# Kernel tuning notes

Measured on AMD Instinct MI355X. Metric: run time of the kernel, lower is better.

The kernel has to match this reference:

```python
import jax, jax.numpy as jnp
import numpy as np

N, C, T, V = 128, 256, 48, 25
CR = C // 16
SEG = 3
BN_EPS = 1e-5


def setup_inputs() -> dict:
    key = jax.random.key(0)
    ks = jax.random.split(key, 8)
    s = lambda k, shape: jax.random.normal(k, shape, dtype=jnp.float32) * 0.05
    return {
        "x": jax.random.normal(ks[0], (N, C, T, V), dtype=jnp.float32),
        "w_sq": s(ks[1], (CR, C)),   # me_squeeze 1x1 conv weight [out,in]
        "b_sq": s(ks[2], (CR,)),
        "gamma": jnp.ones((CR,), jnp.float32),   # BN weight
        "beta": jnp.zeros((CR,), jnp.float32),   # BN bias
        "rmean": jnp.zeros((CR,), jnp.float32),  # BN running mean
        "rvar": jnp.ones((CR,), jnp.float32),    # BN running var
        "w_c1": s(ks[3], (CR, CR)),  # me_conv1 1x1 conv weight
        "b_c1": s(ks[4], (CR,)),
        "w_ex": s(ks[5], (C, CR)),   # me_expand 1x1 conv weight
        "b_ex": s(ks[6], (C,)),
    }


def reference(x, w_sq, b_sq, gamma, beta, rmean, rvar, w_c1, b_c1, w_ex, b_ex):
    n, c, t, v = x.shape
    nb = (n * t) // SEG
    cr = w_sq.shape[0]
    # 1x1 squeeze conv + BatchNorm (eval mode, running stats) -> [n, cr, t, v]
    y = jnp.einsum('nctv,rc->nrtv', x, w_sq) + b_sq[None, :, None, None]
    scale = gamma / jnp.sqrt(rvar + BN_EPS)
    y = y * scale[None, :, None, None] + (beta - rmean * scale)[None, :, None, None]
    # 1x1 conv on squeezed features (shifted branch)
    y1 = jnp.einsum('nrtv,sr->nstv', y, w_c1) + b_c1[None, :, None, None]
    # regroup consecutive frames into segments of SEG along time: (n*t) -> (nb, SEG)
    yseg = y.transpose(0, 2, 1, 3).reshape(nb, SEG, cr, v)
    y1seg = y1.transpose(0, 2, 1, 3).reshape(nb, SEG, cr, v)
    # temporal difference: conv(frame k+1) - frame k, zero-pad last frame of each segment
    diff = y1seg[:, 1:] - yseg[:, :SEG - 1]                    # [nb, SEG-1, cr, v]
    diff = jnp.pad(diff, ((0, 0), (0, 1), (0, 0), (0, 0)))     # [nb, SEG, cr, v]
    x_me = diff.reshape(n, t, cr, v).transpose(0, 2, 1, 3)     # [n, cr, t, v]
    # adaptive avg pool over joints (v -> 1), expand conv, sigmoid gate
    m = jnp.mean(x_me, axis=-1, keepdims=True)                 # [n, cr, t, 1]
    gate = jax.nn.sigmoid(jnp.einsum('nrtu,cr->nctu', m, w_ex) + b_ex[None, :, None, None])
    return x * gate
```

## Files before the change

kernel.cpp:

```cpp
#include <hip/hip_runtime.h>

#define N_  128
#define C_  256
#define T_  48
#define V_  25

typedef float v4f __attribute__((ext_vector_type(4)));

__global__ __launch_bounds__(256) void k_rowmean(const float* __restrict__ x,
                                                 float* __restrict__ xbar) {
    __shared__ float xs[6400];
    const int tid = threadIdx.x;
    const float4* x4 = (const float4*)x;
    const unsigned base4 = blockIdx.x * 1600u;
    #pragma unroll
    for (int k = 0; k < 7; ++k) {
        int i4 = k * 256 + tid;
        if (i4 < 1600) ((float4*)xs)[i4] = x4[base4 + i4];
    }
    __syncthreads();
    float s = 0.f;
    #pragma unroll
    for (int v = 0; v < 25; ++v) s += xs[tid * 25 + v];
    xbar[blockIdx.x * 256u + tid] = s * 0.04f;
}

__global__ __launch_bounds__(512, 4) void k_gateapply(
    const float* __restrict__ x, const float* __restrict__ xbar,
    const float* __restrict__ wsq, const float* __restrict__ bsq,
    const float* __restrict__ gamma, const float* __restrict__ beta,
    const float* __restrict__ rmean, const float* __restrict__ rvar,
    const float* __restrict__ wc1, const float* __restrict__ bc1,
    const float* __restrict__ wex, const float* __restrict__ bex,
    float* __restrict__ out)
{
    __shared__ float xm[12 * 256];
    __shared__ float wsqL[256 * 17];
    __shared__ float gs[256 * 12];
    __shared__ float part[384];
    __shared__ float ybn[192], y1[192], mv[192];

    const int tid = threadIdx.x;
    const unsigned bid = blockIdx.x;
    const unsigned o  = (bid & 7u) * 64u + (bid >> 3);
    const unsigned n  = o >> 2;
    const unsigned qd = o & 3u;

    for (int j = tid; j < 3072; j += 512) {
        int c = j / 12, t = j - c * 12;
        xm[t * 256 + c] = xbar[(unsigned)((n * 256u + c) * 48u + qd * 12u + t)];
    }
    #pragma unroll
    for (int it = 0; it < 8; ++it) {
        int j = it * 512 + tid;
        int r = j >> 8, c = j & 255;
        wsqL[c * 17 + r] = wsq[j];
    }
    __syncthreads();

    if (tid < 384) {
        int t = tid >> 5, rh = tid & 31, r = rh >> 1, h = rh & 1;
        float acc = 0.f;
        #pragma unroll 8
        for (int i = 0; i < 128; ++i)
            acc += xm[t * 256 + h * 128 + i] * wsqL[(h * 128 + i) * 17 + r];
        part[tid] = acc;
    }
    __syncthreads();
    if (tid < 192) {
        int t = tid >> 4, r = tid & 15;
        float acc = part[t * 32 + r * 2] + part[t * 32 + r * 2 + 1];
        float sc = gamma[r] * rsqrtf(rvar[r] + 1e-5f);
        ybn[t * 16 + r] = (acc + bsq[r]) * sc + (beta[r] - rmean[r] * sc);
    }
    __syncthreads();
    if (tid < 192) {
        int t = tid >> 4, s = tid & 15;
        float acc = bc1[s];
        #pragma unroll
        for (int r = 0; r < 16; ++r) acc += ybn[t * 16 + r] * wc1[s * 16 + r];
        y1[t * 16 + s] = acc;
    }
    __syncthreads();
    if (tid < 192) {
        int t = tid >> 4, r = tid & 15;
        mv[tid] = ((t % 3) < 2) ? (y1[(t + 1) * 16 + r] - ybn[t * 16 + r]) : 0.f;
    }
    __syncthreads();
    {
        int c = tid & 255, half = tid >> 8;
        float wexr[16];
        #pragma unroll
        for (int r = 0; r < 16; ++r) wexr[r] = wex[c * 16 + r];
        float be = bex[c];
        #pragma unroll
        for (int t = half * 6; t < half * 6 + 6; ++t) {
            float a = be;
            #pragma unroll
            for (int r = 0; r < 16; ++r) a += mv[t * 16 + r] * wexr[r];
            gs[c * 12 + t] = 1.f / (1.f + expf(-a));
        }
    }
    __syncthreads();

    const v4f* x4 = (const v4f*)x + (size_t)n * 76800u + qd * 75u;
    v4f*       o4 = (v4f*)out     + (size_t)n * 76800u + qd * 75u;
    #pragma unroll 4
    for (int it = 0; it < 38; ++it) {
        int j = it * 512 + tid;
        if (j < 19200) {
            unsigned c = ((unsigned)j * 55926u) >> 22;
            int k = j - (int)c * 75;
            v4f v = x4[c * 300 + k];
            int m0  = k * 4;
            int t0  = (m0 * 41) >> 10;
            int t3  = ((m0 + 3) * 41) >> 10;
            int rem = m0 - t0 * 25;
            float g0 = gs[c * 12 + t0];
            float g3 = gs[c * 12 + t3];
            v4f ov;
            ov.x = v.x * g0;
            ov.y = v.y * ((rem + 1 < 25) ? g0 : g3);
            ov.z = v.z * ((rem + 2 < 25) ? g0 : g3);
            ov.w = v.w * ((rem + 3 < 25) ? g0 : g3);
            __builtin_nontemporal_store(ov, &o4[c * 300 + k]);
        }
    }
}

extern "C" void kernel_launch(void* const* d_in, const int* in_sizes, int n_in,
                              void* d_out, int out_size, void* d_ws, size_t ws_size,
                              hipStream_t stream) {
    const float* x     = (const float*)d_in[0];
    const float* wsq   = (const float*)d_in[1];
    const float* bsq   = (const float*)d_in[2];
    const float* gamma = (const float*)d_in[3];
    const float* beta  = (const float*)d_in[4];
    const float* rmean = (const float*)d_in[5];
    const float* rvar  = (const float*)d_in[6];
    const float* wc1   = (const float*)d_in[7];
    const float* bc1   = (const float*)d_in[8];
    const float* wex   = (const float*)d_in[9];
    const float* bex   = (const float*)d_in[10];

    float* xbar = (float*)d_ws;

    k_rowmean<<<6144, 256, 0, stream>>>(x, xbar);
    k_gateapply<<<512, 512, 0, stream>>>(x, xbar, wsq, bsq, gamma, beta,
                                         rmean, rvar, wc1, bc1, wex, bex,
                                         (float*)d_out);
}
```

Measured before the change: 87.40 us.

## Fuse row-mean and gate-apply into one cooperative kernel with grid sync

Replaces the separate row-mean and gate-apply kernels with a single cooperative kernel of 512 blocks. Each block first computes the joint means for six chunks of x, then a grid-wide sync precedes the original gate computation and apply. Shared memory moves to a dynamic 51200-byte buffer that both phases reuse. This removes one kernel launch and the gap between launches. In exchange it adds a grid barrier, and the 50 KB of shared memory per block may limit how many blocks fit on each CU.

After: 147.4 us. 68.7% more time.

```diff
diff --git a/kernel.cpp b/kernel.cpp
--- a/kernel.cpp
+++ b/kernel.cpp
@@ -1,48 +1,57 @@
 #include <hip/hip_runtime.h>
+#include <hip/hip_cooperative_groups.h>
 
 #define N_  128
 #define C_  256
 #define T_  48
 #define V_  25
 
+namespace cg = cooperative_groups;
 typedef float v4f __attribute__((ext_vector_type(4)));
 
-__global__ __launch_bounds__(256) void k_rowmean(const float* __restrict__ x,
-                                                 float* __restrict__ xbar) {
-    __shared__ float xs[6400];
-    const int tid = threadIdx.x;
-    const float4* x4 = (const float4*)x;
-    const unsigned base4 = blockIdx.x * 1600u;
-    #pragma unroll
-    for (int k = 0; k < 7; ++k) {
-        int i4 = k * 256 + tid;
-        if (i4 < 1600) ((float4*)xs)[i4] = x4[base4 + i4];
-    }
-    __syncthreads();
-    float s = 0.f;
-    #pragma unroll
-    for (int v = 0; v < 25; ++v) s += xs[tid * 25 + v];
-    xbar[blockIdx.x * 256u + tid] = s * 0.04f;
-}
-
-__global__ __launch_bounds__(512, 4) void k_gateapply(
-    const float* __restrict__ x, const float* __restrict__ xbar,
+__global__ __launch_bounds__(512, 4) void k_coop(
+    const float* __restrict__ x,
     const float* __restrict__ wsq, const float* __restrict__ bsq,
     const float* __restrict__ gamma, const float* __restrict__ beta,
     const float* __restrict__ rmean, const float* __restrict__ rvar,
     const float* __restrict__ wc1, const float* __restrict__ bc1,
     const float* __restrict__ wex, const float* __restrict__ bex,
-    float* __restrict__ out)
+    float* __restrict__ xbar, float* __restrict__ out)
 {
-    __shared__ float xm[12 * 256];
-    __shared__ float wsqL[256 * 17];
-    __shared__ float gs[256 * 12];
-    __shared__ float part[384];
-    __shared__ float ybn[192], y1[192], mv[192];
-
+    extern __shared__ float S[];
     const int tid = threadIdx.x;
     const unsigned bid = blockIdx.x;
-    const unsigned o  = (bid & 7u) * 64u + (bid >> 3);
+    const unsigned o   = (bid & 7u) * 64u + (bid >> 3);
+
+    {
+        const v4f* x4 = (const v4f*)x;
+        float* xs = S;
+        for (int ch = 0; ch < 6; ++ch) {
+            const unsigned g4 = (o * 6u + ch) * 3200u;
+            #pragma unroll
+            for (int i = 0; i < 7; ++i) {
+                int j = i * 512 + tid;
+                if (j < 3200) ((v4f*)xs)[j] = x4[g4 + j];
+            }
+            __syncthreads();
+            const float* row = xs + tid * 25;
+            float s = 0.f;
+            #pragma unroll
+            for (int v = 0; v < 25; ++v) s += row[v];
+            xbar[(o * 6u + ch) * 512u + tid] = s * 0.04f;
+            __syncthreads();
+        }
+    }
+    cg::this_grid().sync();
+
+    float* xm   = S;
+    float* wsqL = S + 3072;
+    float* gs   = S + 7424;
+    float* part = S + 10496;
+    float* ybn  = S + 10880;
+    float* y1   = S + 11072;
+    float* mv   = S + 11264;
+
     const unsigned n  = o >> 2;
     const unsigned qd = o & 3u;
 
@@ -103,27 +112,29 @@
     }
     __syncthreads();
 
-    const v4f* x4 = (const v4f*)x + (size_t)n * 76800u + qd * 75u;
-    v4f*       o4 = (v4f*)out     + (size_t)n * 76800u + qd * 75u;
-    #pragma unroll 4
-    for (int it = 0; it < 38; ++it) {
-        int j = it * 512 + tid;
-        if (j < 19200) {
-            unsigned c = ((unsigned)j * 55926u) >> 22;
-            int k = j - (int)c * 75;
-            v4f v = x4[c * 300 + k];
-            int m0  = k * 4;
-            int t0  = (m0 * 41) >> 10;
-            int t3  = ((m0 + 3) * 41) >> 10;
-            int rem = m0 - t0 * 25;
-            float g0 = gs[c * 12 + t0];
-            float g3 = gs[c * 12 + t3];
-            v4f ov;
-            ov.x = v.x * g0;
-            ov.y = v.y * ((rem + 1 < 25) ? g0 : g3);
-            ov.z = v.z * ((rem + 2 < 25) ? g0 : g3);
-            ov.w = v.w * ((rem + 3 < 25) ? g0 : g3);
-            __builtin_nontemporal_store(ov, &o4[c * 300 + k]);
+    {
+        const v4f* x4 = (const v4f*)x + (size_t)n * 76800u + qd * 75u;
+        v4f*       o4 = (v4f*)out     + (size_t)n * 76800u + qd * 75u;
+        #pragma unroll 4
+        for (int it = 0; it < 38; ++it) {
+            int j = it * 512 + tid;
+            if (j < 19200) {
+                unsigned c = ((unsigned)j * 55926u) >> 22;
+                int k = j - (int)c * 75;
+                v4f v = x4[c * 300 + k];
+                int m0  = k * 4;
+                int t0  = (m0 * 41) >> 10;
+                int t3  = ((m0 + 3) * 41) >> 10;
+                int rem = m0 - t0 * 25;
+                float g0 = gs[c * 12 + t0];
+                float g3 = gs[c * 12 + t3];
+                v4f ov;
+                ov.x = v.x * g0;
+                ov.y = v.y * ((rem + 1 < 25) ? g0 : g3);
+                ov.z = v.z * ((rem + 2 < 25) ? g0 : g3);
+                ov.w = v.w * ((rem + 3 < 25) ? g0 : g3);
+                __builtin_nontemporal_store(ov, &o4[c * 300 + k]);
+            }
         }
     }
 }
@@ -142,11 +153,13 @@
     const float* bc1   = (const float*)d_in[8];
     const float* wex   = (const float*)d_in[9];
     const float* bex   = (const float*)d_in[10];
+    float* xbar = (float*)d_ws;
+    float* outp = (float*)d_out;
 
-    float* xbar = (float*)d_ws;
-
-    k_rowmean<<<6144, 256, 0, stream>>>(x, xbar);
-    k_gateapply<<<512, 512, 0, stream>>>(x, xbar, wsq, bsq, gamma, beta,
-                                         rmean, rvar, wc1, bc1, wex, bex,
-                                         (float*)d_out);
+    void* args[] = { (void*)&x, (void*)&wsq, (void*)&bsq, (void*)&gamma,
+                     (void*)&beta, (void*)&rmean, (void*)&rvar, (void*)&wc1,
+                     (void*)&bc1, (void*)&wex, (void*)&bex,
+                     (void*)&xbar, (void*)&outp };
+    hipLaunchCooperativeKernel((const void*)k_coop, dim3(512), dim3(512),
+                               args, 51200, stream);
 }
```

## Fuse row-mean into gate kernel with warp-specialized segment pipeline

Applied to the files above, without the earlier changes.

Removes the separate row-mean kernel and its workspace round trip. Each block now handles four 3-frame segments in turn: half the waves reduce the next segment's joint sums while the other half apply the gate to the previous segment. The goal is to drop one launch and the extra pass that writes and rereads xbar, and to overlap the x reads for the reduction with the gated writes. The cost is more barriers and only half the threads streaming x at any time. Unaligned segment edges are handled with scalar accesses.

New measurement: 134.1 us. +53.4%, slower.

```diff
diff --git a/kernel.cpp b/kernel.cpp
--- a/kernel.cpp
+++ b/kernel.cpp
@@ -1,32 +1,74 @@
 #include <hip/hip_runtime.h>
-
-#define N_  128
-#define C_  256
-#define T_  48
-#define V_  25
 
 typedef float v4f __attribute__((ext_vector_type(4)));
 
-__global__ __launch_bounds__(256) void k_rowmean(const float* __restrict__ x,
-                                                 float* __restrict__ xbar) {
-    __shared__ float xs[6400];
-    const int tid = threadIdx.x;
-    const float4* x4 = (const float4*)x;
-    const unsigned base4 = blockIdx.x * 1600u;
-    #pragma unroll
-    for (int k = 0; k < 7; ++k) {
-        int i4 = k * 256 + tid;
-        if (i4 < 1600) ((float4*)xs)[i4] = x4[base4 + i4];
-    }
-    __syncthreads();
-    float s = 0.f;
-    #pragma unroll
-    for (int v = 0; v < 25; ++v) s += xs[tid * 25 + v];
-    xbar[blockIdx.x * 256u + tid] = s * 0.04f;
+__device__ __forceinline__ void addElem(int m, float v, float& a0, float& a1, float& a2) {
+    if (m < 25) a0 += v; else if (m < 50) a1 += v; else a2 += v;
 }
 
-__global__ __launch_bounds__(512, 4) void k_gateapply(
-    const float* __restrict__ x, const float* __restrict__ xbar,
+template<int PRE>
+__device__ __forceinline__ void aPhase(const float* __restrict__ row, float* xb2, int c) {
+    float a0 = 0.f, a1 = 0.f, a2 = 0.f;
+    #pragma unroll
+    for (int m = 0; m < PRE; ++m) a0 += row[m];
+    const v4f* p = (const v4f*)(row + PRE);
+    #pragma unroll
+    for (int k = 0; k < 18; ++k) {
+        v4f v = p[k];
+        const int m0 = PRE + 4 * k;
+        addElem(m0 + 0, v.x, a0, a1, a2);
+        addElem(m0 + 1, v.y, a0, a1, a2);
+        addElem(m0 + 2, v.z, a0, a1, a2);
+        addElem(m0 + 3, v.w, a0, a1, a2);
+    }
+    #pragma unroll
+    for (int m = PRE + 72; m < 75; ++m) a2 += row[m];
+    xb2[0 * 256 + c] = a0; xb2[1 * 256 + c] = a1; xb2[2 * 256 + c] = a2;
+}
+
+template<int I>
+__device__ __forceinline__ void cPhase(const float* __restrict__ xn, float* __restrict__ on,
+                                       const float* gs, unsigned q, int ctid) {
+    constexpr int PRE  = I;
+    constexpr int OFF4 = (I * 75 + PRE) / 4;
+    const v4f* x4 = (const v4f*)xn;
+    v4f*       o4 = (v4f*)on;
+    const unsigned b4 = q * 75u + (unsigned)OFF4;
+    #pragma unroll 3
+    for (int it = 0; it < 18; ++it) {
+        int j = it * 256 + ctid;
+        unsigned c = ((unsigned)j * 3641u) >> 16;
+        int k = j - (int)c * 18;
+        unsigned idx = b4 + c * 300u + (unsigned)k;
+        v4f v = x4[idx];
+        int m0  = PRE + 4 * k;
+        int t0  = (m0 * 41) >> 10;
+        int t3  = ((m0 + 3) * 41) >> 10;
+        int rem = m0 - t0 * 25;
+        float g0 = gs[c * 3 + t0];
+        float g3 = gs[c * 3 + t3];
+        v4f ov;
+        ov.x = v.x * g0;
+        ov.y = v.y * ((rem + 1 < 25) ? g0 : g3);
+        ov.z = v.z * ((rem + 2 < 25) ? g0 : g3);
+        ov.w = v.w * ((rem + 3 < 25) ? g0 : g3);
+        __builtin_nontemporal_store(ov, &o4[idx]);
+    }
+    #pragma unroll
+    for (int it = 0; it < 3; ++it) {
+        int j = it * 256 + ctid;
+        unsigned c = ((unsigned)j * 683u) >> 11;
+        int e = j - (int)c * 3;
+        int m = (e < PRE) ? e : (72 + e);
+        int t = (e < PRE) ? 0 : 2;
+        unsigned fi = c * 1200u + (q * 4u + I) * 75u + (unsigned)m;
+        float val = xn[fi] * gs[c * 3 + t];
+        __builtin_nontemporal_store(val, &on[fi]);
+    }
+}
+
+__global__ __launch_bounds__(512, 4) void k_pipe2(
+    const float* __restrict__ x,
     const float* __restrict__ wsq, const float* __restrict__ bsq,
     const float* __restrict__ gamma, const float* __restrict__ beta,
     const float* __restrict__ rmean, const float* __restrict__ rvar,
@@ -34,98 +76,92 @@
     const float* __restrict__ wex, const float* __restrict__ bex,
     float* __restrict__ out)
 {
-    __shared__ float xm[12 * 256];
-    __shared__ float wsqL[256 * 17];
-    __shared__ float gs[256 * 12];
+    __shared__ float xb2[768];
+    __shared__ float gs[768];
     __shared__ float part[384];
-    __shared__ float ybn[192], y1[192], mv[192];
+    __shared__ float ybn[48], y1[48], mv[48];
 
     const int tid = threadIdx.x;
+    const int wv  = tid >> 6, ln = tid & 63;
     const unsigned bid = blockIdx.x;
-    const unsigned o  = (bid & 7u) * 64u + (bid >> 3);
-    const unsigned n  = o >> 2;
-    const unsigned qd = o & 3u;
+    const unsigned u = (bid & 7u) * 64u + (bid >> 3);
+    const unsigned n = u >> 2;
+    const unsigned q = u & 3u;
 
-    for (int j = tid; j < 3072; j += 512) {
-        int c = j / 12, t = j - c * 12;
-        xm[t * 256 + c] = xbar[(unsigned)((n * 256u + c) * 48u + qd * 12u + t)];
-    }
-    #pragma unroll
-    for (int it = 0; it < 8; ++it) {
-        int j = it * 512 + tid;
-        int r = j >> 8, c = j & 255;
-        wsqL[c * 17 + r] = wsq[j];
-    }
+    const float* xn = x   + (size_t)n * 307200u;
+    float*       on = out + (size_t)n * 307200u;
+    const int ca = (wv >= 4) ? ((wv - 4) * 64 + ln) : 0;
+    const int ct = wv * 64 + ln;
+
+    auto bPhase = [&]() {
+        if (tid < 384) {
+            int g = tid & 7, qq = tid >> 3;
+            int t = qq >> 4, r = qq & 15;
+            float acc = 0.f;
+            #pragma unroll 8
+            for (int i2 = 0; i2 < 32; ++i2) {
+                int c = i2 * 8 + g;
+                acc += xb2[t * 256 + c] * wsq[r * 256 + c];
+            }
+            part[tid] = acc;
+        }
+        __syncthreads();
+        if (tid < 48) {
+            int t = tid >> 4, r = tid & 15;
+            float acc = 0.f;
+            #pragma unroll
+            for (int g = 0; g < 8; ++g) acc += part[(t * 16 + r) * 8 + g];
+            float sc = gamma[r] * rsqrtf(rvar[r] + 1e-5f);
+            ybn[t * 16 + r] = acc * (0.04f * sc) + (bsq[r] * sc + beta[r] - rmean[r] * sc);
+            float yv = bc1[r];
+            #pragma unroll
+            for (int rr = 0; rr < 16; ++rr) yv += ybn[t * 16 + rr] * wc1[r * 16 + rr];
+            y1[t * 16 + r] = yv;
+            mv[t * 16 + r] = (t < 2) ? (y1[(t + 1) * 16 + r] - ybn[t * 16 + r]) : 0.f;
+        }
+        __syncthreads();
+        {
+            int c = tid & 255;
+            float be = bex[c];
+            if (tid < 256) {
+                float a0 = be, a1 = be;
+                #pragma unroll
+                for (int r = 0; r < 16; ++r) {
+                    float w = wex[c * 16 + r];
+                    a0 += mv[r] * w; a1 += mv[16 + r] * w;
+                }
+                gs[c * 3 + 0] = 1.f / (1.f + expf(-a0));
+                gs[c * 3 + 1] = 1.f / (1.f + expf(-a1));
+            } else {
+                float a2 = be;
+                #pragma unroll
+                for (int r = 0; r < 16; ++r) a2 += mv[32 + r] * wex[c * 16 + r];
+                gs[c * 3 + 2] = 1.f / (1.f + expf(-a2));
+            }
+        }
+        __syncthreads();
+    };
+
+    if (wv >= 4) aPhase<0>(xn + ca * 1200 + (q * 4 + 0) * 75, xb2, ca);
     __syncthreads();
 
-    if (tid < 384) {
-        int t = tid >> 5, rh = tid & 31, r = rh >> 1, h = rh & 1;
-        float acc = 0.f;
-        #pragma unroll 8
-        for (int i = 0; i < 128; ++i)
-            acc += xm[t * 256 + h * 128 + i] * wsqL[(h * 128 + i) * 17 + r];
-        part[tid] = acc;
-    }
-    __syncthreads();
-    if (tid < 192) {
-        int t = tid >> 4, r = tid & 15;
-        float acc = part[t * 32 + r * 2] + part[t * 32 + r * 2 + 1];
-        float sc = gamma[r] * rsqrtf(rvar[r] + 1e-5f);
-        ybn[t * 16 + r] = (acc + bsq[r]) * sc + (beta[r] - rmean[r] * sc);
-    }
-    __syncthreads();
-    if (tid < 192) {
-        int t = tid >> 4, s = tid & 15;
-        float acc = bc1[s];
-        #pragma unroll
-        for (int r = 0; r < 16; ++r) acc += ybn[t * 16 + r] * wc1[s * 16 + r];
-        y1[t * 16 + s] = acc;
-    }
-    __syncthreads();
-    if (tid < 192) {
-        int t = tid >> 4, r = tid & 15;
-        mv[tid] = ((t % 3) < 2) ? (y1[(t + 1) * 16 + r] - ybn[t * 16 + r]) : 0.f;
-    }
-    __syncthreads();
-    {
-        int c = tid & 255, half = tid >> 8;
-        float wexr[16];
-        #pragma unroll
-        for (int r = 0; r < 16; ++r) wexr[r] = wex[c * 16 + r];
-        float be = bex[c];
-        #pragma unroll
-        for (int t = half * 6; t < half * 6 + 6; ++t) {
-            float a = be;
-            #pragma unroll
-            for (int r = 0; r < 16; ++r) a += mv[t * 16 + r] * wexr[r];
-            gs[c * 12 + t] = 1.f / (1.f + expf(-a));
-        }
-    }
+    bPhase();
+    if (wv >= 4) aPhase<1>(xn + ca * 1200 + (q * 4 + 1) * 75, xb2, ca);
+    else         cPhase<0>(xn, on, gs, q, ct);
     __syncthreads();
 
-    const v4f* x4 = (const v4f*)x + (size_t)n * 76800u + qd * 75u;
-    v4f*       o4 = (v4f*)out     + (size_t)n * 76800u + qd * 75u;
-    #pragma unroll 4
-    for (int it = 0; it < 38; ++it) {
-        int j = it * 512 + tid;
-        if (j < 19200) {
-            unsigned c = ((unsigned)j * 55926u) >> 22;
-            int k = j - (int)c * 75;
-            v4f v = x4[c * 300 + k];
-            int m0  = k * 4;
-            int t0  = (m0 * 41) >> 10;
-            int t3  = ((m0 + 3) * 41) >> 10;
-            int rem = m0 - t0 * 25;
-            float g0 = gs[c * 12 + t0];
-            float g3 = gs[c * 12 + t3];
-            v4f ov;
-            ov.x = v.x * g0;
-            ov.y = v.y * ((rem + 1 < 25) ? g0 : g3);
-            ov.z = v.z * ((rem + 2 < 25) ? g0 : g3);
-            ov.w = v.w * ((rem + 3 < 25) ? g0 : g3);
-            __builtin_nontemporal_store(ov, &o4[c * 300 + k]);
-        }
-    }
+    bPhase();
+    if (wv >= 4) aPhase<2>(xn + ca * 1200 + (q * 4 + 2) * 75, xb2, ca);
+    else         cPhase<1>(xn, on, gs, q, ct);
+    __syncthreads();
+
+    bPhase();
+    if (wv >= 4) aPhase<3>(xn + ca * 1200 + (q * 4 + 3) * 75, xb2, ca);
+    else         cPhase<2>(xn, on, gs, q, ct);
+    __syncthreads();
+
+    bPhase();
+    if (wv < 4) cPhase<3>(xn, on, gs, q, ct);
 }
 
 extern "C" void kernel_launch(void* const* d_in, const int* in_sizes, int n_in,
@@ -143,10 +179,7 @@
     const float* wex   = (const float*)d_in[9];
     const float* bex   = (const float*)d_in[10];
 
-    float* xbar = (float*)d_ws;
-
-    k_rowmean<<<6144, 256, 0, stream>>>(x, xbar);
-    k_gateapply<<<512, 512, 0, stream>>>(x, xbar, wsq, bsq, gamma, beta,
-                                         rmean, rvar, wc1, bc1, wex, bex,
-                                         (float*)d_out);
+    k_pipe2<<<512, 512, 0, stream>>>(x, wsq, bsq, gamma, beta,
+                                     rmean, rvar, wc1, bc1, wex, bex,
+                                     (float*)d_out);
 }
```

## Fuse rowmean and gating into one warp-specialized kernel with bf16 LDS staging

Applied to the files above, without the earlier changes.

Replaces the two-kernel flow (row means written to workspace, then gate plus apply re-reading x) with a single kernel. Each block handles half a sample, loops over 3-frame segments, and stages x into double-buffered shared memory as bf16. Half the waves load the next segment while the other half compute the gate and write out the current one, so x is read from global memory only once. The output is now x rounded to bf16 times the gate, which loses precision relative to the fp32 reference. The grid is also cut to 256 blocks, and the many barriers per segment may limit overlap.

Result: slower. 160.9 us (+84.1%).

```diff
diff --git a/kernel.cpp b/kernel.cpp
--- a/kernel.cpp
+++ b/kernel.cpp
@@ -1,32 +1,22 @@
 #include <hip/hip_runtime.h>
 
-#define N_  128
-#define C_  256
-#define T_  48
-#define V_  25
+typedef float v4f __attribute__((ext_vector_type(4)));
+typedef unsigned int u32;
+typedef unsigned short u16;
 
-typedef float v4f __attribute__((ext_vector_type(4)));
+#define STR 76
 
-__global__ __launch_bounds__(256) void k_rowmean(const float* __restrict__ x,
-                                                 float* __restrict__ xbar) {
-    __shared__ float xs[6400];
-    const int tid = threadIdx.x;
-    const float4* x4 = (const float4*)x;
-    const unsigned base4 = blockIdx.x * 1600u;
-    #pragma unroll
-    for (int k = 0; k < 7; ++k) {
-        int i4 = k * 256 + tid;
-        if (i4 < 1600) ((float4*)xs)[i4] = x4[base4 + i4];
-    }
-    __syncthreads();
-    float s = 0.f;
-    #pragma unroll
-    for (int v = 0; v < 25; ++v) s += xs[tid * 25 + v];
-    xbar[blockIdx.x * 256u + tid] = s * 0.04f;
+__device__ __forceinline__ float b2f(u16 u) {
+    union { float f; u32 i; } c; c.i = ((u32)u) << 16; return c.f;
+}
+__device__ __forceinline__ u16 f2b(float f) {
+    union { float f; u32 i; } c; c.f = f;
+    u32 r = c.i + 0x7fffu + ((c.i >> 16) & 1u);
+    return (u16)(r >> 16);
 }
 
-__global__ __launch_bounds__(512, 4) void k_gateapply(
-    const float* __restrict__ x, const float* __restrict__ xbar,
+__global__ __launch_bounds__(512, 2) void k_ws(
+    const float* __restrict__ x,
     const float* __restrict__ wsq, const float* __restrict__ bsq,
     const float* __restrict__ gamma, const float* __restrict__ beta,
     const float* __restrict__ rmean, const float* __restrict__ rvar,
@@ -34,97 +24,156 @@
     const float* __restrict__ wex, const float* __restrict__ bex,
     float* __restrict__ out)
 {
-    __shared__ float xm[12 * 256];
-    __shared__ float wsqL[256 * 17];
-    __shared__ float gs[256 * 12];
+    __shared__ u16   buf[2][256 * STR];
+    __shared__ float xb[768];
+    __shared__ float gs[768];
     __shared__ float part[384];
-    __shared__ float ybn[192], y1[192], mv[192];
+    __shared__ float ybn[48], y1[48], mv[48];
 
-    const int tid = threadIdx.x;
+    const int tid  = threadIdx.x;
+    const int wv   = tid >> 6;
+    const int atid = tid & 255;
     const unsigned bid = blockIdx.x;
-    const unsigned o  = (bid & 7u) * 64u + (bid >> 3);
-    const unsigned n  = o >> 2;
-    const unsigned qd = o & 3u;
+    const unsigned o    = (bid & 7u) * 32u + (bid >> 3);
+    const unsigned n    = o >> 1;
+    const unsigned half = o & 1u;
 
-    for (int j = tid; j < 3072; j += 512) {
-        int c = j / 12, t = j - c * 12;
-        xm[t * 256 + c] = xbar[(unsigned)((n * 256u + c) * 48u + qd * 12u + t)];
-    }
-    #pragma unroll
-    for (int it = 0; it < 8; ++it) {
-        int j = it * 512 + tid;
-        int r = j >> 8, c = j & 255;
-        wsqL[c * 17 + r] = wsq[j];
-    }
-    __syncthreads();
+    const float* xn = x   + (size_t)n * 307200u + half * 600u;
+    float*       on = out + (size_t)n * 307200u + half * 600u;
 
-    if (tid < 384) {
-        int t = tid >> 5, rh = tid & 31, r = rh >> 1, h = rh & 1;
-        float acc = 0.f;
-        #pragma unroll 8
-        for (int i = 0; i < 128; ++i)
-            acc += xm[t * 256 + h * 128 + i] * wsqL[(h * 128 + i) * 17 + r];
-        part[tid] = acc;
-    }
-    __syncthreads();
-    if (tid < 192) {
-        int t = tid >> 4, r = tid & 15;
-        float acc = part[t * 32 + r * 2] + part[t * 32 + r * 2 + 1];
-        float sc = gamma[r] * rsqrtf(rvar[r] + 1e-5f);
-        ybn[t * 16 + r] = (acc + bsq[r]) * sc + (beta[r] - rmean[r] * sc);
-    }
-    __syncthreads();
-    if (tid < 192) {
-        int t = tid >> 4, s = tid & 15;
-        float acc = bc1[s];
+    auto stageA = [&](int i, int h) {
+        u16* B = buf[i & 1];
+        const float* sb = xn + i * 75;
         #pragma unroll
-        for (int r = 0; r < 16; ++r) acc += ybn[t * 16 + r] * wc1[s * 16 + r];
-        y1[t * 16 + s] = acc;
-    }
-    __syncthreads();
-    if (tid < 192) {
-        int t = tid >> 4, r = tid & 15;
-        mv[tid] = ((t % 3) < 2) ? (y1[(t + 1) * 16 + r] - ybn[t * 16 + r]) : 0.f;
-    }
-    __syncthreads();
-    {
-        int c = tid & 255, half = tid >> 8;
-        float wexr[16];
+        for (int it = 0; it < 18; ++it) {
+            int j = it * 256 + atid;
+            int c = j / 18, k = j - c * 18;
+            v4f v = *(const v4f*)(sb + c * 1200 + h + 4 * k);
+            u32 p0 = (u32)f2b(v.x) | ((u32)f2b(v.y) << 16);
+            u32 p1 = (u32)f2b(v.z) | ((u32)f2b(v.w) << 16);
+            u32 s = (u32)(c * STR + 4 * k);
+            *(u32*)&B[s]     = p0;
+            *(u32*)&B[s + 2] = p1;
+        }
         #pragma unroll
-        for (int r = 0; r < 16; ++r) wexr[r] = wex[c * 16 + r];
-        float be = bex[c];
+        for (int it = 0; it < 3; ++it) {
+            int j = it * 256 + atid;
+            int c = j / 3, e = j - c * 3;
+            int m = (e < h) ? e : e + 72;
+            B[c * STR + 72 + e] = f2b(sb[c * 1200 + m]);
+        }
+    };
+
+    auto applyD = [&](int i, int h) {
+        const u16* B = buf[i & 1];
+        float* ob = on + i * 75;
         #pragma unroll
-        for (int t = half * 6; t < half * 6 + 6; ++t) {
-            float a = be;
-            #pragma unroll
-            for (int r = 0; r < 16; ++r) a += mv[t * 16 + r] * wexr[r];
-            gs[c * 12 + t] = 1.f / (1.f + expf(-a));
-        }
-    }
-    __syncthreads();
-
-    const v4f* x4 = (const v4f*)x + (size_t)n * 76800u + qd * 75u;
-    v4f*       o4 = (v4f*)out     + (size_t)n * 76800u + qd * 75u;
-    #pragma unroll 4
-    for (int it = 0; it < 38; ++it) {
-        int j = it * 512 + tid;
-        if (j < 19200) {
-            unsigned c = ((unsigned)j * 55926u) >> 22;
-            int k = j - (int)c * 75;
-            v4f v = x4[c * 300 + k];
-            int m0  = k * 4;
+        for (int it = 0; it < 18; ++it) {
+            int j = it * 256 + atid;
+            int c = j / 18, k = j - c * 18;
+            u32 s  = (u32)(c * STR + 4 * k);
+            u32 q0 = *(const u32*)&B[s];
+            u32 q1 = *(const u32*)&B[s + 2];
+            int m0  = h + 4 * k;
             int t0  = (m0 * 41) >> 10;
             int t3  = ((m0 + 3) * 41) >> 10;
             int rem = m0 - t0 * 25;
-            float g0 = gs[c * 12 + t0];
-            float g3 = gs[c * 12 + t3];
+            float g0 = gs[c * 3 + t0];
+            float g3 = gs[c * 3 + t3];
             v4f ov;
-            ov.x = v.x * g0;
-            ov.y = v.y * ((rem + 1 < 25) ? g0 : g3);
-            ov.z = v.z * ((rem + 2 < 25) ? g0 : g3);
-            ov.w = v.w * ((rem + 3 < 25) ? g0 : g3);
-            __builtin_nontemporal_store(ov, &o4[c * 300 + k]);
+            ov.x = b2f((u16)(q0 & 0xffffu)) * g0;
+            ov.y = b2f((u16)(q0 >> 16))     * ((rem + 1 < 25) ? g0 : g3);
+            ov.z = b2f((u16)(q1 & 0xffffu)) * ((rem + 2 < 25) ? g0 : g3);
+            ov.w = b2f((u16)(q1 >> 16))     * ((rem + 3 < 25) ? g0 : g3);
+            __builtin_nontemporal_store(ov, (v4f*)(ob + c * 1200 + h + 4 * k));
         }
+        #pragma unroll
+        for (int it = 0; it < 3; ++it) {
+            int j = it * 256 + atid;
+            int c = j / 3, e = j - c * 3;
+            int m = (e < h) ? e : e + 72;
+            int t = (e < h) ? 0 : 2;
+            float val = b2f(B[c * STR + 72 + e]) * gs[c * 3 + t];
+            __builtin_nontemporal_store(val, ob + c * 1200 + m);
+        }
+    };
+
+    auto bPhase = [&](int i, int h) {
+        const u16* B = buf[i & 1];
+        for (int p = tid; p < 768; p += 512) {
+            int c = p & 255, t = p >> 8;
+            float s = 0.f;
+            #pragma unroll
+            for (int v = 0; v < 25; ++v) {
+                int m  = t * 25 + v;
+                int sl = (m >= h && m < h + 72) ? (m - h) : ((m < h) ? 72 + m : m);
+                s += b2f(B[c * STR + sl]);
+            }
+            xb[t * 256 + c] = s;
+        }
+        __syncthreads();
+        if (tid < 384) {
+            int g = tid & 7, q = tid >> 3, t = q >> 4, r = q & 15;
+            float acc = 0.f;
+            #pragma unroll 8
+            for (int ii = 0; ii < 32; ++ii) {
+                int c = g * 32 + ii;
+                acc += xb[t * 256 + c] * wsq[r * 256 + c];
+            }
+            part[tid] = acc;
+        }
+        __syncthreads();
+        if (tid < 48) {
+            int t = tid >> 4, r = tid & 15;
+            float acc = 0.f;
+            #pragma unroll
+            for (int g = 0; g < 8; ++g) acc += part[((t * 16 + r) << 3) + g];
+            float sc = gamma[r] * rsqrtf(rvar[r] + 1e-5f);
+            ybn[tid] = acc * (0.04f * sc) + (bsq[r] * sc + beta[r] - rmean[r] * sc);
+        }
+        __syncthreads();
+        if (tid < 48) {
+            int t = tid >> 4, s = tid & 15;
+            float acc = bc1[s];
+            #pragma unroll
+            for (int r = 0; r < 16; ++r) acc += ybn[t * 16 + r] * wc1[s * 16 + r];
+            y1[tid] = acc;
+        }
+        __syncthreads();
+        if (tid < 48) {
+            int t = tid >> 4;
+            mv[tid] = (t < 2) ? (y1[tid + 16] - ybn[tid]) : 0.f;
+        }
+        __syncthreads();
+        if (tid < 256) {
+            int c = tid;
+            float be = bex[c];
+            float a0 = be, a1 = be, a2 = be;
+            #pragma unroll
+            for (int r = 0; r < 16; ++r) {
+                float w = wex[c * 16 + r];
+                a0 += mv[r] * w; a1 += mv[16 + r] * w; a2 += mv[32 + r] * w;
+            }
+            gs[c * 3 + 0] = 1.f / (1.f + expf(-a0));
+            gs[c * 3 + 1] = 1.f / (1.f + expf(-a1));
+            gs[c * 3 + 2] = 1.f / (1.f + expf(-a2));
+        }
+        __syncthreads();
+    };
+
+    if (wv >= 4) stageA(0, 0);
+    __syncthreads();
+
+    #pragma unroll
+    for (int i = 0; i < 8; ++i) {
+        const int h = i & 3;
+        bPhase(i, h);
+        if (wv >= 4) {
+            if (i < 7) stageA(i + 1, (i + 1) & 3);
+        } else {
+            applyD(i, h);
+        }
+        __syncthreads();
     }
 }
 
@@ -143,10 +192,7 @@
     const float* wex   = (const float*)d_in[9];
     const float* bex   = (const float*)d_in[10];
 
-    float* xbar = (float*)d_ws;
-
-    k_rowmean<<<6144, 256, 0, stream>>>(x, xbar);
-    k_gateapply<<<512, 512, 0, stream>>>(x, xbar, wsq, bsq, gamma, beta,
-                                         rmean, rvar, wc1, bc1, wex, bex,
-                                         (float*)d_out);
+    k_ws<<<256, 512, 0, stream>>>(x, wsq, bsq, gamma, beta,
+                                  rmean, rvar, wc1, bc1, wex, bex,
+                                  (float*)d_out);
 }
```
